# Kernel tuning notes

Measured on AMD Instinct MI355X. Metric: run time of the kernel, lower is better.

The kernel has to match this reference:

```python
import jax, jax.numpy as jnp
import numpy as np

TOP_K = 8
N_GROUP = 8
TOPK_GROUP = 4
ROUTED_SCALING_FACTOR = 2.5
NORM_TOPK_PROB = True
TOKENS = 16384
HIDDEN = 4096
N_EXPERTS = 256


def setup_inputs() -> dict:
    key = jax.random.key(0)
    k1, k2, k3 = jax.random.split(key, 3)
    x = jax.random.normal(k1, (TOKENS, HIDDEN), dtype=jnp.float32)
    weight = jax.random.normal(k2, (N_EXPERTS, HIDDEN), dtype=jnp.float32) * 0.02
    e_score_correction_bias = jax.random.normal(k3, (N_EXPERTS,), dtype=jnp.float32) * 0.01
    return {"x": x, "weight": weight, "e_score_correction_bias": e_score_correction_bias}


def reference(x, weight, e_score_correction_bias):
    # gates: [T, E]
    gates = x @ weight.T
    orig_scores = jax.nn.sigmoid(gates.astype(jnp.float32))
    scores = orig_scores + e_score_correction_bias
    T, E = scores.shape
    eg = E // N_GROUP  # experts per group
    s = scores.reshape(T, N_GROUP, eg)
    # group score = sum of top-2 expert scores within each group -> [T, G]
    group_scores = jax.lax.top_k(s, 2)[0].sum(axis=-1)
    # torch code selects the (n_group - topk_group) SMALLEST groups and keeps
    # only those (masked_fill zeroes everything else) -- replicate faithfully.
    k_drop = N_GROUP - TOPK_GROUP
    _, bottom_idx = jax.lax.top_k(-group_scores, k_drop)  # [T, k_drop]
    keep = jnp.zeros((T, N_GROUP), dtype=bool).at[jnp.arange(T)[:, None], bottom_idx].set(True)
    s = jnp.where(keep[:, :, None], s, 0.0).reshape(T, E)
    # torch.topk(-scores) -> indices of the k SMALLEST scores
    _, inds = jax.lax.top_k(-s, TOP_K)  # [T, top_k]
    sel = jnp.take_along_axis(orig_scores, inds, axis=-1)
    if TOP_K > 1 and NORM_TOPK_PROB:
        sel = sel / (sel.sum(axis=-1, keepdims=True) + 1e-20)
    sel = sel * ROUTED_SCALING_FACTOR
    return inds, sel
```

## Files before the change

### kernel.cpp

```cpp
#include <hip/hip_runtime.h>
#include <hip/hip_fp16.h>
#include <cstdint>
#include <cmath>

#define TOKENS  16384
#define HIDDEN  4096
#define NEXP    256
#define TOPK    8
#define KDROP   4

typedef _Float16 f16x8  __attribute__((ext_vector_type(8)));
typedef _Float16 f16x4  __attribute__((ext_vector_type(4)));
typedef float    f32x16 __attribute__((ext_vector_type(16)));
typedef float    f32x4  __attribute__((ext_vector_type(4)));

#define LO_SCALE 2048.0f
#define LO_INV   (1.0f/2048.0f)

#define WS_G0_OFF 0
#define WS_G1_OFF 16777216
#define WS_WH_OFF 33554432
#define WS_WL_OFF 35651584

__global__ __launch_bounds__(256)
void wsplit(const float* __restrict__ w, _Float16* __restrict__ wh,
            _Float16* __restrict__ wl)
{
    const int idx = blockIdx.x * 256 + threadIdx.x;
    const int e   = idx >> 9;
    const int kg8 = idx & 511;
    const float4* p = (const float4*)(w + (size_t)e * HIDDEN + kg8 * 8);
    float4 f0 = p[0], f1 = p[1];
    float v[8] = {f0.x, f0.y, f0.z, f0.w, f1.x, f1.y, f1.z, f1.w};
    f16x8 hi, lo;
    #pragma unroll
    for (int i = 0; i < 8; ++i) {
        _Float16 h = (_Float16)v[i];
        hi[i] = h;
        lo[i] = (_Float16)((v[i] - (float)h) * LO_SCALE);
    }
    const int kc = kg8 >> 2, s = (kg8 >> 1) & 1, hl = kg8 & 1;
    const int cid = ((kc * 2 + s) * 8 + (e >> 5)) * 64 + hl * 32 + (e & 31);
    ((f16x8*)wh)[cid] = hi;
    ((f16x8*)wl)[cid] = lo;
}

__global__ __launch_bounds__(512, 4)
void gemm_split(const float* __restrict__ x, const _Float16* __restrict__ wh,
                const _Float16* __restrict__ wl,
                float* __restrict__ g0, float* __restrict__ g1)
{
    __shared__ _Float16 Ah[2][64 * 32];
    __shared__ _Float16 Al[2][64 * 32];

    const int tid  = threadIdx.x;
    const int w    = tid >> 6;
    const int lane = tid & 63;

    const int bid  = blockIdx.x;
    const int y    = bid & 1;
    const int tok0 = (bid >> 1) * 64;
    const int kcg0 = y * 64;
    float* gates_half = y ? g1 : g0;

    const int srow = (tid >> 1) & 31;
    const int shl  = (tid >> 6) & 1;
    const int sr   = (tid >> 7) & 1;
    const int ss   = (tid >> 8) & 1;
    const int stok = sr * 32 + srow;
    const int sk   = ss * 16 + shl * 8 + (tid & 1) * 4;
    const float* xr = x + (size_t)(tok0 + stok) * HIDDEN + (size_t)kcg0 * 32 + sk;

    const f16x8* whc = (const f16x8*)wh;
    const f16x8* wlc = (const f16x8*)wl;

    f32x16 accH[2] = {};
    f32x16 accX[2] = {};

    f16x8 bh[2], bl[2];
    f32x4 aM;

    {
        f32x4 a0 = *(const f32x4*)(xr);
        aM = *(const f32x4*)(xr + 32);
        #pragma unroll
        for (int s = 0; s < 2; ++s) {
            bh[s] = whc[((kcg0 * 2 + s) * 8 + w) * 64 + lane];
            bl[s] = wlc[((kcg0 * 2 + s) * 8 + w) * 64 + lane];
        }
        f16x4 hi, lo;
        #pragma unroll
        for (int i = 0; i < 4; ++i) {
            _Float16 h = (_Float16)a0[i];
            hi[i] = h;
            lo[i] = (_Float16)((a0[i] - (float)h) * LO_SCALE);
        }
        *(f16x4*)&Ah[0][tid * 4] = hi;
        *(f16x4*)&Al[0][tid * 4] = lo;
    }
    __syncthreads();

    #pragma unroll 2
    for (int kc = 0; kc < 64; ++kc) {
        const int cur = kc & 1;

        f32x4 aN;
        f16x8 bhn[2], bln[2];
        if (kc + 2 < 64) {
            aN = *(const f32x4*)(xr + (kc + 2) * 32);
        }
        if (kc + 1 < 64) {
            const int kcg = kcg0 + kc + 1;
            #pragma unroll
            for (int s = 0; s < 2; ++s) {
                bhn[s] = whc[((kcg * 2 + s) * 8 + w) * 64 + lane];
                bln[s] = wlc[((kcg * 2 + s) * 8 + w) * 64 + lane];
            }
        }

        #pragma unroll
        for (int s = 0; s < 2; ++s) {
            f16x8 ah0 = *(const f16x8*)&Ah[cur][((s * 2 + 0) * 64 + lane) * 8];
            f16x8 ah1 = *(const f16x8*)&Ah[cur][((s * 2 + 1) * 64 + lane) * 8];
            f16x8 al0 = *(const f16x8*)&Al[cur][((s * 2 + 0) * 64 + lane) * 8];
            f16x8 al1 = *(const f16x8*)&Al[cur][((s * 2 + 1) * 64 + lane) * 8];

            accH[0] = __builtin_amdgcn_mfma_f32_32x32x16_f16(ah0, bh[s], accH[0], 0, 0, 0);
            accH[1] = __builtin_amdgcn_mfma_f32_32x32x16_f16(ah1, bh[s], accH[1], 0, 0, 0);
            accX[0] = __builtin_amdgcn_mfma_f32_32x32x16_f16(al0, bh[s], accX[0], 0, 0, 0);
            accX[1] = __builtin_amdgcn_mfma_f32_32x32x16_f16(al1, bh[s], accX[1], 0, 0, 0);
            accX[0] = __builtin_amdgcn_mfma_f32_32x32x16_f16(ah0, bl[s], accX[0], 0, 0, 0);
            accX[1] = __builtin_amdgcn_mfma_f32_32x32x16_f16(ah1, bl[s], accX[1], 0, 0, 0);
        }

        if (kc + 1 < 64) {
            f16x4 hi, lo;
            #pragma unroll
            for (int i = 0; i < 4; ++i) {
                _Float16 h = (_Float16)aM[i];
                hi[i] = h;
                lo[i] = (_Float16)((aM[i] - (float)h) * LO_SCALE);
            }
            *(f16x4*)&Ah[cur ^ 1][tid * 4] = hi;
            *(f16x4*)&Al[cur ^ 1][tid * 4] = lo;
            aM = aN;
            #pragma unroll
            for (int s = 0; s < 2; ++s) {
                bh[s] = bhn[s];
                bl[s] = bln[s];
            }
        }
        __syncthreads();
    }

    const int col   = lane & 31;
    const int rbase = 4 * (lane >> 5);
    #pragma unroll
    for (int r = 0; r < 2; ++r) {
        float* gp = gates_half + (size_t)(tok0 + r * 32) * NEXP + w * 32 + col;
        #pragma unroll
        for (int reg = 0; reg < 16; ++reg) {
            const int row = (reg & 3) + 8 * (reg >> 2) + rbase;
            gp[(size_t)row * NEXP] = accH[r][reg] + accX[r][reg] * LO_INV;
        }
    }
}

__device__ __forceinline__ unsigned ordkey(float f) {
    unsigned u = __float_as_uint(f);
    return (u & 0x80000000u) ? ~u : (u | 0x80000000u);
}

__global__ __launch_bounds__(256, 4)
void gate_epilogue(const float* __restrict__ g0,
                   const float* __restrict__ g1,
                   const float* __restrict__ bias,
                   float* __restrict__ out)
{
    const int tid  = threadIdx.x;
    const int wv   = tid >> 6;
    const int lane = tid & 63;
    const int t    = blockIdx.x * 4 + wv;

    float4 ga = ((const float4*)(g0 + (size_t)t * NEXP))[lane];
    float4 gb = ((const float4*)(g1 + (size_t)t * NEXP))[lane];
    float4 bv = ((const float4*)bias)[lane];
    float4 gv = make_float4(ga.x + gb.x, ga.y + gb.y, ga.z + gb.z, ga.w + gb.w);

    float sig0 = 1.0f / (1.0f + expf(-gv.x));
    float sig1 = 1.0f / (1.0f + expf(-gv.y));
    float sig2 = 1.0f / (1.0f + expf(-gv.z));
    float sig3 = 1.0f / (1.0f + expf(-gv.w));
    float sc0 = sig0 + bv.x, sc1 = sig1 + bv.y;
    float sc2 = sig2 + bv.z, sc3 = sig3 + bv.w;

    float m1 = fmaxf(sc0, sc1);
    float m2 = fminf(sc0, sc1);
    if (sc2 > m1) { m2 = m1; m1 = sc2; } else m2 = fmaxf(m2, sc2);
    if (sc3 > m1) { m2 = m1; m1 = sc3; } else m2 = fmaxf(m2, sc3);
    #pragma unroll
    for (int off = 1; off < 8; off <<= 1) {
        float o1 = __shfl_xor(m1, off);
        float o2 = __shfl_xor(m2, off);
        float nm1 = fmaxf(m1, o1);
        float nm2 = fmaxf(fminf(m1, o1), fmaxf(m2, o2));
        m1 = nm1; m2 = nm2;
    }
    float gsum = m1 + m2;
    float gs[8];
    #pragma unroll
    for (int gi = 0; gi < 8; ++gi) gs[gi] = __shfl(gsum, gi * 8);

    int keepmask = 0;
    #pragma unroll
    for (int g = 0; g < 8; ++g) {
        int rank = 0;
        #pragma unroll
        for (int h = 0; h < 8; ++h)
            rank += (gs[h] < gs[g]) || (gs[h] == gs[g] && h < g);
        if (rank < KDROP) keepmask |= (1 << g);
    }
    const bool kept = (keepmask >> (lane >> 3)) & 1;

    const unsigned ib = (unsigned)(lane * 4);
    unsigned long long k0 = ((unsigned long long)ordkey(kept ? sc0 : 0.0f) << 32) | (ib + 0);
    unsigned long long k1 = ((unsigned long long)ordkey(kept ? sc1 : 0.0f) << 32) | (ib + 1);
    unsigned long long k2 = ((unsigned long long)ordkey(kept ? sc2 : 0.0f) << 32) | (ib + 2);
    unsigned long long k3 = ((unsigned long long)ordkey(kept ? sc3 : 0.0f) << 32) | (ib + 3);

    float ssum = 0.0f, myval = 0.0f;
    int myidx = 0;
    #pragma unroll
    for (int r = 0; r < TOPK; ++r) {
        unsigned long long kmin = k0 < k1 ? k0 : k1;
        if (k2 < kmin) kmin = k2;
        if (k3 < kmin) kmin = k3;
        #pragma unroll
        for (int off = 32; off >= 1; off >>= 1) {
            unsigned long long o = __shfl_xor(kmin, off);
            if (o < kmin) kmin = o;
        }
        const int id   = (int)(kmin & 0xffffffffull);
        const int src  = id >> 2;
        const int slot = id & 3;
        float vsrc = (slot == 0) ? sig0 : (slot == 1) ? sig1
                   : (slot == 2) ? sig2 : sig3;
        float v = __shfl(vsrc, src);
        ssum += v;
        if (lane == r) { myidx = id; myval = v; }
        const bool mine = (lane == src);
        if (mine && slot == 0) k0 = ~0ull;
        if (mine && slot == 1) k1 = ~0ull;
        if (mine && slot == 2) k2 = ~0ull;
        if (mine && slot == 3) k3 = ~0ull;
    }

    if (lane < TOPK) {
        out[(size_t)t * TOPK + lane] = (float)myidx;
        out[(size_t)TOKENS * TOPK + (size_t)t * TOPK + lane] =
            myval / (ssum + 1e-20f) * 2.5f;
    }
}

extern "C" void kernel_launch(void* const* d_in, const int* in_sizes, int n_in,
                              void* d_out, int out_size, void* d_ws, size_t ws_size,
                              hipStream_t stream)
{
    const float* x    = (const float*)d_in[0];
    const float* w    = (const float*)d_in[1];
    const float* bias = (const float*)d_in[2];
    float* out = (float*)d_out;

    float*     g0 = (float*)((char*)d_ws + WS_G0_OFF);
    float*     g1 = (float*)((char*)d_ws + WS_G1_OFF);
    _Float16*  wh = (_Float16*)((char*)d_ws + WS_WH_OFF);
    _Float16*  wl = (_Float16*)((char*)d_ws + WS_WL_OFF);

    wsplit<<<dim3(512), dim3(256), 0, stream>>>(w, wh, wl);
    gemm_split<<<dim3(512), dim3(512), 0, stream>>>(x, wh, wl, g0, g1);
    gate_epilogue<<<dim3(TOKENS / 4), dim3(256), 0, stream>>>(g0, g1, bias, out);
}
```

Measured before the change: 481.2 us.

## Stage fp32 activations via direct global-to-LDS loads and split experts across blocks

The GEMM now copies raw fp32 activation tiles straight into LDS with global_load_lds and does the hi/lo fp16 split after reading from LDS, instead of converting in registers before the LDS store. Each block is halved to 256 threads covering 128 experts, so there are twice as many blocks. Weight fragments are loaded for the current k-chunk instead of being prefetched one chunk ahead, and MFMA sections are raised to high priority with s_setprio. The goal is to cut register pressure and VGPR round-trips for activation staging. The cost is that each x tile is now read by two blocks, the split arithmetic is repeated per wave, and weight load latency is no longer hidden by prefetch.

```diff
diff --git a/kernel.cpp b/kernel.cpp
--- a/kernel.cpp
+++ b/kernel.cpp
@@ -10,7 +10,6 @@
 #define KDROP   4
 
 typedef _Float16 f16x8  __attribute__((ext_vector_type(8)));
-typedef _Float16 f16x4  __attribute__((ext_vector_type(4)));
 typedef float    f32x16 __attribute__((ext_vector_type(16)));
 typedef float    f32x4  __attribute__((ext_vector_type(4)));
 
@@ -21,6 +20,13 @@
 #define WS_G1_OFF 16777216
 #define WS_WH_OFF 33554432
 #define WS_WL_OFF 35651584
+
+static __device__ __forceinline__ void gload16(const float* g, float* l)
+{
+    __builtin_amdgcn_global_load_lds(
+        (const __attribute__((address_space(1))) unsigned int*)g,
+        (__attribute__((address_space(3))) unsigned int*)l, 16, 0, 0);
+}
 
 __global__ __launch_bounds__(256)
 void wsplit(const float* __restrict__ w, _Float16* __restrict__ wh,
@@ -45,13 +51,12 @@
     ((f16x8*)wl)[cid] = lo;
 }
 
-__global__ __launch_bounds__(512, 4)
+__global__ __launch_bounds__(256, 4)
 void gemm_split(const float* __restrict__ x, const _Float16* __restrict__ wh,
                 const _Float16* __restrict__ wl,
                 float* __restrict__ g0, float* __restrict__ g1)
 {
-    __shared__ _Float16 Ah[2][64 * 32];
-    __shared__ _Float16 Al[2][64 * 32];
+    __shared__ float A32[2][2048];
 
     const int tid  = threadIdx.x;
     const int w    = tid >> 6;
@@ -59,17 +64,18 @@
 
     const int bid  = blockIdx.x;
     const int y    = bid & 1;
-    const int tok0 = (bid >> 1) * 64;
+    const int eh   = (bid >> 1) & 1;
+    const int tok0 = (bid >> 2) * 64;
     const int kcg0 = y * 64;
+    const int we   = eh * 4 + w;
     float* gates_half = y ? g1 : g0;
 
-    const int srow = (tid >> 1) & 31;
-    const int shl  = (tid >> 6) & 1;
+    const int sl   = tid & 63;
+    const int sjh  = (tid >> 6) & 1;
     const int sr   = (tid >> 7) & 1;
-    const int ss   = (tid >> 8) & 1;
-    const int stok = sr * 32 + srow;
-    const int sk   = ss * 16 + shl * 8 + (tid & 1) * 4;
-    const float* xr = x + (size_t)(tok0 + stok) * HIDDEN + (size_t)kcg0 * 32 + sk;
+    const int stok = sr * 32 + (sl & 31);
+    const int koff = ((sl >> 5)) * 8 + sjh * 4;
+    const float* xb = x + (size_t)(tok0 + stok) * HIDDEN + (size_t)kcg0 * 32 + koff;
 
     const f16x8* whc = (const f16x8*)wh;
     const f16x8* wlc = (const f16x8*)wl;
@@ -77,79 +83,65 @@
     f32x16 accH[2] = {};
     f32x16 accX[2] = {};
 
-    f16x8 bh[2], bl[2];
-    f32x4 aM;
-
-    {
-        f32x4 a0 = *(const f32x4*)(xr);
-        aM = *(const f32x4*)(xr + 32);
-        #pragma unroll
-        for (int s = 0; s < 2; ++s) {
-            bh[s] = whc[((kcg0 * 2 + s) * 8 + w) * 64 + lane];
-            bl[s] = wlc[((kcg0 * 2 + s) * 8 + w) * 64 + lane];
-        }
-        f16x4 hi, lo;
-        #pragma unroll
-        for (int i = 0; i < 4; ++i) {
-            _Float16 h = (_Float16)a0[i];
-            hi[i] = h;
-            lo[i] = (_Float16)((a0[i] - (float)h) * LO_SCALE);
-        }
-        *(f16x4*)&Ah[0][tid * 4] = hi;
-        *(f16x4*)&Al[0][tid * 4] = lo;
-    }
+    gload16(xb,      &A32[0][tid * 4]);
+    gload16(xb + 16, &A32[0][(tid + 256) * 4]);
+    asm volatile("s_waitcnt vmcnt(0)" ::: "memory");
     __syncthreads();
 
     #pragma unroll 2
     for (int kc = 0; kc < 64; ++kc) {
         const int cur = kc & 1;
 
-        f32x4 aN;
-        f16x8 bhn[2], bln[2];
-        if (kc + 2 < 64) {
-            aN = *(const f32x4*)(xr + (kc + 2) * 32);
-        }
         if (kc + 1 < 64) {
-            const int kcg = kcg0 + kc + 1;
+            const float* gp = xb + (size_t)(kc + 1) * 32;
+            gload16(gp,      &A32[cur ^ 1][tid * 4]);
+            gload16(gp + 16, &A32[cur ^ 1][(tid + 256) * 4]);
+        }
+
+        f16x8 bh[2], bl[2];
+        {
+            const int kcg = kcg0 + kc;
             #pragma unroll
             for (int s = 0; s < 2; ++s) {
-                bhn[s] = whc[((kcg * 2 + s) * 8 + w) * 64 + lane];
-                bln[s] = wlc[((kcg * 2 + s) * 8 + w) * 64 + lane];
+                bh[s] = whc[((kcg * 2 + s) * 8 + we) * 64 + lane];
+                bl[s] = wlc[((kcg * 2 + s) * 8 + we) * 64 + lane];
             }
         }
 
         #pragma unroll
         for (int s = 0; s < 2; ++s) {
-            f16x8 ah0 = *(const f16x8*)&Ah[cur][((s * 2 + 0) * 64 + lane) * 8];
-            f16x8 ah1 = *(const f16x8*)&Ah[cur][((s * 2 + 1) * 64 + lane) * 8];
-            f16x8 al0 = *(const f16x8*)&Al[cur][((s * 2 + 0) * 64 + lane) * 8];
-            f16x8 al1 = *(const f16x8*)&Al[cur][((s * 2 + 1) * 64 + lane) * 8];
-
+            f16x8 ah0, al0, ah1, al1;
+            #pragma unroll
+            for (int r = 0; r < 2; ++r) {
+                f32x4 u0 = *(const f32x4*)&A32[cur][(((s * 2 + r) * 2 + 0) * 64 + lane) * 4];
+                f32x4 u1 = *(const f32x4*)&A32[cur][(((s * 2 + r) * 2 + 1) * 64 + lane) * 4];
+                f16x8 hi, lo;
+                #pragma unroll
+                for (int i = 0; i < 4; ++i) {
+                    _Float16 h = (_Float16)u0[i];
+                    hi[i] = h;
+                    lo[i] = (_Float16)((u0[i] - (float)h) * LO_SCALE);
+                }
+                #pragma unroll
+                for (int i = 0; i < 4; ++i) {
+                    _Float16 h = (_Float16)u1[i];
+                    hi[i + 4] = h;
+                    lo[i + 4] = (_Float16)((u1[i] - (float)h) * LO_SCALE);
+                }
+                if (r == 0) { ah0 = hi; al0 = lo; }
+                else        { ah1 = hi; al1 = lo; }
+            }
+
+            __builtin_amdgcn_s_setprio(1);
             accH[0] = __builtin_amdgcn_mfma_f32_32x32x16_f16(ah0, bh[s], accH[0], 0, 0, 0);
             accH[1] = __builtin_amdgcn_mfma_f32_32x32x16_f16(ah1, bh[s], accH[1], 0, 0, 0);
             accX[0] = __builtin_amdgcn_mfma_f32_32x32x16_f16(al0, bh[s], accX[0], 0, 0, 0);
             accX[1] = __builtin_amdgcn_mfma_f32_32x32x16_f16(al1, bh[s], accX[1], 0, 0, 0);
             accX[0] = __builtin_amdgcn_mfma_f32_32x32x16_f16(ah0, bl[s], accX[0], 0, 0, 0);
             accX[1] = __builtin_amdgcn_mfma_f32_32x32x16_f16(ah1, bl[s], accX[1], 0, 0, 0);
-        }
-
-        if (kc + 1 < 64) {
-            f16x4 hi, lo;
-            #pragma unroll
-            for (int i = 0; i < 4; ++i) {
-                _Float16 h = (_Float16)aM[i];
-                hi[i] = h;
-                lo[i] = (_Float16)((aM[i] - (float)h) * LO_SCALE);
-            }
-            *(f16x4*)&Ah[cur ^ 1][tid * 4] = hi;
-            *(f16x4*)&Al[cur ^ 1][tid * 4] = lo;
-            aM = aN;
-            #pragma unroll
-            for (int s = 0; s < 2; ++s) {
-                bh[s] = bhn[s];
-                bl[s] = bln[s];
-            }
-        }
+            __builtin_amdgcn_s_setprio(0);
+        }
+
         __syncthreads();
     }
 
@@ -157,7 +149,7 @@
     const int rbase = 4 * (lane >> 5);
     #pragma unroll
     for (int r = 0; r < 2; ++r) {
-        float* gp = gates_half + (size_t)(tok0 + r * 32) * NEXP + w * 32 + col;
+        float* gp = gates_half + (size_t)(tok0 + r * 32) * NEXP + eh * 128 + w * 32 + col;
         #pragma unroll
         for (int reg = 0; reg < 16; ++reg) {
             const int row = (reg & 3) + 8 * (reg >> 2) + rbase;
@@ -277,6 +269,6 @@
     _Float16*  wl = (_Float16*)((char*)d_ws + WS_WL_OFF);
 
     wsplit<<<dim3(512), dim3(256), 0, stream>>>(w, wh, wl);
-    gemm_split<<<dim3(512), dim3(512), 0, stream>>>(x, wh, wl, g0, g1);
+    gemm_split<<<dim3(1024), dim3(256), 0, stream>>>(x, wh, wl, g0, g1);
     gate_epilogue<<<dim3(TOKENS / 4), dim3(256), 0, stream>>>(g0, g1, bias, out);
 }
```

New measurement: 487.9 us. No clear change (+1.4%).
